# Kernel optimization log

Hardware: AMD Instinct MI355X
Metric: run time of the kernel (lower is better)

Reference implementation:

```python
import jax, jax.numpy as jnp
import numpy as np


def setup_inputs() -> dict:
    key = jax.random.key(0)
    k1, k2, k3, k4 = jax.random.split(key, 4)
    B, D_vis, E, N = 512, 4096, 1024, 512
    vf = jax.random.normal(k1, (B, D_vis), dtype=jnp.float32)
    p_lfs = jax.random.normal(k2, (B, E), dtype=jnp.float32)
    n_lfs = jax.random.normal(k3, (N, E), dtype=jnp.float32)
    W = jax.random.normal(k4, (E, D_vis), dtype=jnp.float32) * (1.0 / np.sqrt(D_vis))
    b = jnp.zeros((E,), dtype=jnp.float32)
    return {"vf": vf, "p_lfs": p_lfs, "n_lfs": n_lfs, "W": W, "b": b}


def _partial_order_sim(hypers, hypos):
    # -||relu(hypers - hypos)||_2 along last dim
    act = jax.nn.relu(hypers - hypos)
    return -jnp.sqrt(jnp.sum(act * act, axis=-1))


def reference(vf, p_lfs, n_lfs, W, b):
    # vf: [B, D_vis], W: [E, D_vis] -> vf_emb: [B, E]
    vf_emb = jnp.einsum("bd,ed->be", vf, W) + b
    # positive scores: [B]
    p_scores = _partial_order_sim(p_lfs, vf_emb)
    # negative scores, batched over B: n_lfs [N,E] vs vf_emb [B,E] -> [B,N]
    n_scores = _partial_order_sim(n_lfs[None, :, :], vf_emb[:, None, :])
    # score_stack: [B, 1+N]
    return jnp.concatenate([p_scores[:, None], n_scores], axis=1)
```

## Files before the change

kernel.cpp:

```cpp
#include <hip/hip_runtime.h>
#include <hip/hip_bf16.h>

constexpr int B = 512;
constexpr int D = 4096;
constexpr int E = 1024;
constexpr int N = 512;
constexpr int KSW = 16;
constexpr int KSG = 4;
constexpr int KC = D / KSW;
constexpr int NSTEP = KC / 32;
constexpr int ES = 8;
constexpr int EC = E / ES;
constexpr int DEPTH = 2;

typedef __attribute__((ext_vector_type(8))) short bf16x8;
typedef __attribute__((ext_vector_type(4))) float f32x4;
typedef _Float16 h2 __attribute__((ext_vector_type(2)));
typedef _Float16 h4 __attribute__((ext_vector_type(4)));
typedef _Float16 h8 __attribute__((ext_vector_type(8)));

typedef __attribute__((address_space(3))) void lds_void;
typedef const __attribute__((address_space(1))) void gbl_void;

__device__ __forceinline__ unsigned short f2bf(float f) {
    __hip_bfloat16 h = __float2bfloat16(f);
    return *reinterpret_cast<unsigned short*>(&h);
}

#if __has_builtin(__builtin_amdgcn_fdot2)
__device__ __forceinline__ float fdot2(h2 a, h2 b, float c) {
    return __builtin_amdgcn_fdot2(a, b, c, false);
}
#else
__device__ __forceinline__ float fdot2(h2 a, h2 b, float c) {
    return c + (float)a[0] * (float)b[0] + (float)a[1] * (float)b[1];
}
#endif

__global__ __launch_bounds__(256) void cvt_all(
    const float* __restrict__ vf, const float* __restrict__ W,
    const float* __restrict__ n_lfs,
    unsigned short* __restrict__ vfB, unsigned short* __restrict__ WB,
    _Float16* __restrict__ n16)
{
    const int bid = blockIdx.x;
    if (bid < 3072) {
        const float* src;
        unsigned short* dst;
        int i;
        if (bid < 1024) { src = vf; dst = vfB; i = (bid * 256 + threadIdx.x) * 8; }
        else           { src = W;  dst = WB;  i = ((bid - 1024) * 256 + threadIdx.x) * 8; }
        float4 v0 = *(const float4*)(src + i);
        float4 v1 = *(const float4*)(src + i + 4);
        bf16x8 o;
        o[0] = (short)f2bf(v0.x); o[1] = (short)f2bf(v0.y);
        o[2] = (short)f2bf(v0.z); o[3] = (short)f2bf(v0.w);
        o[4] = (short)f2bf(v1.x); o[5] = (short)f2bf(v1.y);
        o[6] = (short)f2bf(v1.z); o[7] = (short)f2bf(v1.w);
        *(bf16x8*)(dst + i) = o;
    } else {
        const int i = ((bid - 3072) * 256 + threadIdx.x) * 8;
        float4 v0 = *(const float4*)(n_lfs + i);
        float4 v1 = *(const float4*)(n_lfs + i + 4);
        h8 o;
        o[0] = (_Float16)v0.x; o[1] = (_Float16)v0.y;
        o[2] = (_Float16)v0.z; o[3] = (_Float16)v0.w;
        o[4] = (_Float16)v1.x; o[5] = (_Float16)v1.y;
        o[6] = (_Float16)v1.z; o[7] = (_Float16)v1.w;
        *(h8*)(n16 + i) = o;
    }
}

__global__ __launch_bounds__(256) void gemm_lds(
    const unsigned short* __restrict__ vf,
    const unsigned short* __restrict__ W,
    _Float16* __restrict__ part)
{
    __shared__ __align__(16) char smem[70656];

    const int t = threadIdx.x;
    const int w = t >> 6;
    const int L = t & 63;

    const int id = blockIdx.x + 16 * blockIdx.y + 128 * blockIdx.z;
    const int l  = (id & 7) * 64 + (id >> 3);
    const int z  = l >> 7;
    const int n0 = (l & 15) * 64;
    const int m0 = ((l >> 4) & 7) * 64;

    char* stg = smem + w * 16384;

    const int subrow = L >> 2;
    const int qstg = (L & 3) ^ ((L >> 2) & 3) ^ ((L >> 4) & 3);
    const int kbeg = (z * 4 + w) * KC;
    const unsigned short* aSrc[4];
    const unsigned short* bSrc[4];
    #pragma unroll
    for (int c = 0; c < 4; ++c) {
        aSrc[c] = vf + (size_t)(m0 + c * 16 + subrow) * D + kbeg + qstg * 8;
        bSrc[c] = W  + (size_t)(n0 + c * 16 + subrow) * D + kbeg + qstg * 8;
    }

    const int r16 = L & 15;
    const int quad = L >> 4;
    const int swz = quad ^ (r16 & 3) ^ ((r16 >> 2) & 3);
    const int aoff = r16 * 64 + swz * 16;

    f32x4 acc[4][4] = {};

    auto issue = [&](int step, int buf) {
        const size_t koff = (size_t)step * 32;
        #pragma unroll
        for (int c = 0; c < 4; ++c) {
            __builtin_amdgcn_global_load_lds(
                (gbl_void*)(aSrc[c] + koff),
                (lds_void*)(stg + buf * 4096 + c * 1024), 16, 0, 0);
            __builtin_amdgcn_global_load_lds(
                (gbl_void*)(bSrc[c] + koff),
                (lds_void*)(stg + 8192 + buf * 4096 + c * 1024), 16, 0, 0);
        }
    };

    issue(0, 0);
    issue(1, 1);

    #define GSTEP(S, WC, ISS)                                                  \
    {                                                                          \
        const int buf_ = (S) & 1;                                              \
        __builtin_amdgcn_s_waitcnt(WC);                                        \
        bf16x8 af[4], bg[4];                                                   \
        _Pragma("unroll")                                                      \
        for (int i = 0; i < 4; ++i)                                            \
            af[i] = *(const bf16x8*)(stg + buf_ * 4096 + i * 1024 + aoff);     \
        _Pragma("unroll")                                                      \
        for (int j = 0; j < 4; ++j)                                            \
            bg[j] = *(const bf16x8*)(stg + 8192 + buf_ * 4096 + j * 1024 + aoff); \
        _Pragma("unroll")                                                      \
        for (int i = 0; i < 4; ++i)                                            \
            _Pragma("unroll")                                                  \
            for (int j = 0; j < 4; ++j)                                        \
                acc[i][j] = __builtin_amdgcn_mfma_f32_16x16x32_bf16(           \
                    af[i], bg[j], acc[i][j], 0, 0, 0);                         \
        if (ISS) issue((S) + DEPTH, buf_);                                     \
    }

    #pragma unroll 1
    for (int s = 0; s < NSTEP - 1; ++s)
        GSTEP(s, 0x0F78, s + DEPTH < NSTEP);
    GSTEP(NSTEP - 1, 0x0F70, false);
    #undef GSTEP

    __syncthreads();
    float* ctw = (float*)smem + w * 4416;
    #pragma unroll
    for (int i = 0; i < 4; ++i)
        #pragma unroll
        for (int j = 0; j < 4; ++j)
            #pragma unroll
            for (int r = 0; r < 4; ++r)
                ctw[(i * 16 + quad * 4 + r) * 69 + (j * 16 + r16)] = acc[i][j][r];
    __syncthreads();

    const int row = t >> 2;
    const int cb  = (t & 3) * 16;
    const float* p0 = (const float*)smem + row * 69 + cb;
    float s[16];
    #pragma unroll
    for (int u = 0; u < 16; ++u)
        s[u] = (p0[u] + p0[4416 + u]) + (p0[8832 + u] + p0[13248 + u]);
    _Float16* po = part + (size_t)z * B * E + (size_t)(m0 + row) * E + n0 + cb;
    h8 v0, v1;
    #pragma unroll
    for (int u = 0; u < 8; ++u) { v0[u] = (_Float16)s[u]; v1[u] = (_Float16)s[u + 8]; }
    *(h8*)po = v0;
    *(h8*)(po + 8) = v1;
}

__global__ __launch_bounds__(256) void reduce_emb(
    const _Float16* __restrict__ part, const float* __restrict__ bias,
    const float* __restrict__ p_lfs,
    _Float16* __restrict__ emb16, float* __restrict__ out)
{
    const int b = blockIdx.x;
    const int e = threadIdx.x * 4;
    const size_t base = (size_t)b * E + e;
    float4 s = *(const float4*)(bias + e);
    #pragma unroll
    for (int ks = 0; ks < KSG; ++ks) {
        h4 p = *(const h4*)(part + (size_t)ks * B * E + base);
        s.x += (float)p[0]; s.y += (float)p[1];
        s.z += (float)p[2]; s.w += (float)p[3];
    }
    h4 o;
    o[0] = (_Float16)s.x; o[1] = (_Float16)s.y;
    o[2] = (_Float16)s.z; o[3] = (_Float16)s.w;
    *(h4*)(emb16 + base) = o;

    const float4 pl = *(const float4*)(p_lfs + base);
    float d, a = 0.f;
    d = pl.x - s.x; d = fmaxf(d, 0.f); a = fmaf(d, d, a);
    d = pl.y - s.y; d = fmaxf(d, 0.f); a = fmaf(d, d, a);
    d = pl.z - s.z; d = fmaxf(d, 0.f); a = fmaf(d, d, a);
    d = pl.w - s.w; d = fmaxf(d, 0.f); a = fmaf(d, d, a);
    #pragma unroll
    for (int off = 32; off; off >>= 1) a += __shfl_down(a, off, 64);
    __shared__ float red[4];
    if ((threadIdx.x & 63) == 0) red[threadIdx.x >> 6] = a;
    __syncthreads();
    if (threadIdx.x == 0)
        out[(size_t)b * 513] = -sqrtf(red[0] + red[1] + red[2] + red[3]);
}

__global__ __launch_bounds__(256, 4) void scores_part(
    const _Float16* __restrict__ emb16,
    const _Float16* __restrict__ n16,
    _Float16* __restrict__ pn)
{
    constexpr int LDH = EC + 8;
    __shared__ _Float16 eS[64 * LDH];
    __shared__ _Float16 nS[64 * LDH];

    const int t  = threadIdx.x;
    const int n0 = blockIdx.x * 64;
    const int b0 = blockIdx.y * 64;
    const int e0 = blockIdx.z * EC;

    {
        const int row = t >> 2;
        const int cb  = (t & 3) * 32;
        const _Float16* ep = emb16 + (size_t)(b0 + row) * E + e0 + cb;
        const _Float16* np = n16   + (size_t)(n0 + row) * E + e0 + cb;
        _Float16* ed = &eS[row * LDH + cb];
        _Float16* nd = &nS[row * LDH + cb];
        #pragma unroll
        for (int q = 0; q < 4; ++q) {
            h8 v = *(const h8*)(ep + q * 8);
            h8 w = *(const h8*)(np + q * 8);
            *(h8*)(ed + q * 8) = -v;
            *(h8*)(nd + q * 8) = w;
        }
    }
    __syncthreads();

    const int ty = t >> 4;
    const int tx = t & 15;

    float acc[4][4] = {};
    const h4 z4 = {};

    #pragma unroll 2
    for (int e = 0; e < EC; e += 4) {
        h4 a[4], c[4];
        #pragma unroll
        for (int r = 0; r < 4; ++r)
            a[r] = *(const h4*)&eS[(ty + 16 * r) * LDH + e];
        #pragma unroll
        for (int q = 0; q < 4; ++q)
            c[q] = *(const h4*)&nS[(tx + 16 * q) * LDH + e];
        #pragma unroll
        for (int r = 0; r < 4; ++r)
            #pragma unroll
            for (int q = 0; q < 4; ++q) {
                h4 d = c[q] + a[r];
                d = __builtin_elementwise_max(d, z4);
                h2 dl = __builtin_shufflevector(d, d, 0, 1);
                h2 dh = __builtin_shufflevector(d, d, 2, 3);
                acc[r][q] = fdot2(dl, dl, acc[r][q]);
                acc[r][q] = fdot2(dh, dh, acc[r][q]);
            }
    }

    _Float16* po = pn + (size_t)blockIdx.z * B * N;
    #pragma unroll
    for (int r = 0; r < 4; ++r) {
        const size_t ob = (size_t)(b0 + ty + 16 * r) * N;
        #pragma unroll
        for (int q = 0; q < 4; ++q)
            po[ob + n0 + tx + 16 * q] = (_Float16)acc[r][q];
    }
}

__global__ __launch_bounds__(256) void scores_final(
    const _Float16* __restrict__ pn,
    float* __restrict__ out)
{
    const int i = blockIdx.x * 256 + threadIdx.x;
    const int b = i >> 9;
    const int n = i & (N - 1);
    float s = 0.f;
    #pragma unroll
    for (int z = 0; z < ES; ++z)
        s += (float)pn[(size_t)z * B * N + i];
    out[(size_t)b * 513 + 1 + n] = -sqrtf(s);
}

extern "C" void kernel_launch(void* const* d_in, const int* in_sizes, int n_in,
                              void* d_out, int out_size, void* d_ws, size_t ws_size,
                              hipStream_t stream) {
    const float* vf    = (const float*)d_in[0];
    const float* p_lfs = (const float*)d_in[1];
    const float* n_lfs = (const float*)d_in[2];
    const float* W     = (const float*)d_in[3];
    const float* bias  = (const float*)d_in[4];
    float* out = (float*)d_out;

    char* ws = (char*)d_ws;
    _Float16*       pg    = (_Float16*)ws;
    _Float16*       pn    = (_Float16*)(ws + ((size_t)4 << 20));
    unsigned short* vfB   = (unsigned short*)(ws + ((size_t)8 << 20));
    unsigned short* WB    = (unsigned short*)(ws + ((size_t)12 << 20));
    _Float16*       emb16 = (_Float16*)(ws + ((size_t)20 << 20));
    _Float16*       n16   = (_Float16*)(ws + ((size_t)21 << 20));

    cvt_all<<<3328, 256, 0, stream>>>(vf, W, n_lfs, vfB, WB, n16);

    dim3 g1(E / 64, B / 64, KSG);
    gemm_lds<<<g1, 256, 0, stream>>>(vfB, WB, pg);

    reduce_emb<<<B, 256, 0, stream>>>(pg, bias, p_lfs, emb16, out);

    dim3 g3(N / 64, B / 64, ES);
    scores_part<<<g3, 256, 0, stream>>>(emb16, n16, pn);

    scores_final<<<(B * N) / 256, 256, 0, stream>>>(pn, out);
}
```

Measured before the change: 113.4 us.

## Fuse split-K reduction and positive scores into GEMM, convert n_lfs in scores kernel

```diff
diff --git a/kernel.cpp b/kernel.cpp
--- a/kernel.cpp
+++ b/kernel.cpp
@@ -5,9 +5,7 @@
 constexpr int D = 4096;
 constexpr int E = 1024;
 constexpr int N = 512;
-constexpr int KSW = 16;
-constexpr int KSG = 4;
-constexpr int KC = D / KSW;
+constexpr int KC = 512;
 constexpr int NSTEP = KC / 32;
 constexpr int ES = 8;
 constexpr int EC = E / ES;
@@ -39,86 +37,83 @@
 
 __global__ __launch_bounds__(256) void cvt_all(
     const float* __restrict__ vf, const float* __restrict__ W,
-    const float* __restrict__ n_lfs,
     unsigned short* __restrict__ vfB, unsigned short* __restrict__ WB,
-    _Float16* __restrict__ n16)
+    float* __restrict__ psum)
 {
     const int bid = blockIdx.x;
-    if (bid < 3072) {
-        const float* src;
-        unsigned short* dst;
-        int i;
-        if (bid < 1024) { src = vf; dst = vfB; i = (bid * 256 + threadIdx.x) * 8; }
-        else           { src = W;  dst = WB;  i = ((bid - 1024) * 256 + threadIdx.x) * 8; }
-        float4 v0 = *(const float4*)(src + i);
-        float4 v1 = *(const float4*)(src + i + 4);
-        bf16x8 o;
-        o[0] = (short)f2bf(v0.x); o[1] = (short)f2bf(v0.y);
-        o[2] = (short)f2bf(v0.z); o[3] = (short)f2bf(v0.w);
-        o[4] = (short)f2bf(v1.x); o[5] = (short)f2bf(v1.y);
-        o[6] = (short)f2bf(v1.z); o[7] = (short)f2bf(v1.w);
-        *(bf16x8*)(dst + i) = o;
-    } else {
-        const int i = ((bid - 3072) * 256 + threadIdx.x) * 8;
-        float4 v0 = *(const float4*)(n_lfs + i);
-        float4 v1 = *(const float4*)(n_lfs + i + 4);
-        h8 o;
-        o[0] = (_Float16)v0.x; o[1] = (_Float16)v0.y;
-        o[2] = (_Float16)v0.z; o[3] = (_Float16)v0.w;
-        o[4] = (_Float16)v1.x; o[5] = (_Float16)v1.y;
-        o[6] = (_Float16)v1.z; o[7] = (_Float16)v1.w;
-        *(h8*)(n16 + i) = o;
-    }
-}
-
-__global__ __launch_bounds__(256) void gemm_lds(
+    if (bid == 3072) {
+        if (threadIdx.x < 128)
+            ((f32x4*)psum)[threadIdx.x] = (f32x4){0.f, 0.f, 0.f, 0.f};
+        return;
+    }
+    const float* src;
+    unsigned short* dst;
+    int i;
+    if (bid < 1024) { src = vf; dst = vfB; i = (bid * 256 + threadIdx.x) * 8; }
+    else           { src = W;  dst = WB;  i = ((bid - 1024) * 256 + threadIdx.x) * 8; }
+    float4 v0 = *(const float4*)(src + i);
+    float4 v1 = *(const float4*)(src + i + 4);
+    bf16x8 o;
+    o[0] = (short)f2bf(v0.x); o[1] = (short)f2bf(v0.y);
+    o[2] = (short)f2bf(v0.z); o[3] = (short)f2bf(v0.w);
+    o[4] = (short)f2bf(v1.x); o[5] = (short)f2bf(v1.y);
+    o[6] = (short)f2bf(v1.z); o[7] = (short)f2bf(v1.w);
+    *(bf16x8*)(dst + i) = o;
+}
+
+__global__ __launch_bounds__(512, 2) void gemm_fused(
     const unsigned short* __restrict__ vf,
     const unsigned short* __restrict__ W,
-    _Float16* __restrict__ part)
+    const float* __restrict__ bias,
+    const float* __restrict__ p_lfs,
+    _Float16* __restrict__ emb16,
+    float* __restrict__ psum)
 {
-    __shared__ __align__(16) char smem[70656];
+    __shared__ __align__(16) char smem[98304];
 
     const int t = threadIdx.x;
     const int w = t >> 6;
     const int L = t & 63;
 
-    const int id = blockIdx.x + 16 * blockIdx.y + 128 * blockIdx.z;
-    const int l  = (id & 7) * 64 + (id >> 3);
-    const int z  = l >> 7;
-    const int n0 = (l & 15) * 64;
-    const int m0 = ((l >> 4) & 7) * 64;
-
-    char* stg = smem + w * 16384;
+    const int id  = blockIdx.x;
+    const int xcd = id & 7;
+    const int w8  = id >> 3;
+    const int m0 = ((xcd >> 2) * 8 + (w8 & 7)) * 32;
+    const int n0 = ((xcd & 3) * 4 + (w8 >> 3)) * 64;
+
+    char* stg = smem + w * 12288;
 
     const int subrow = L >> 2;
     const int qstg = (L & 3) ^ ((L >> 2) & 3) ^ ((L >> 4) & 3);
-    const int kbeg = (z * 4 + w) * KC;
-    const unsigned short* aSrc[4];
+    const int kbeg = w * KC;
+    const unsigned short* aSrc[2];
     const unsigned short* bSrc[4];
     #pragma unroll
-    for (int c = 0; c < 4; ++c) {
+    for (int c = 0; c < 2; ++c)
         aSrc[c] = vf + (size_t)(m0 + c * 16 + subrow) * D + kbeg + qstg * 8;
+    #pragma unroll
+    for (int c = 0; c < 4; ++c)
         bSrc[c] = W  + (size_t)(n0 + c * 16 + subrow) * D + kbeg + qstg * 8;
-    }
 
     const int r16 = L & 15;
     const int quad = L >> 4;
     const int swz = quad ^ (r16 & 3) ^ ((r16 >> 2) & 3);
     const int aoff = r16 * 64 + swz * 16;
 
-    f32x4 acc[4][4] = {};
+    f32x4 acc[2][4] = {};
 
     auto issue = [&](int step, int buf) {
         const size_t koff = (size_t)step * 32;
         #pragma unroll
-        for (int c = 0; c < 4; ++c) {
+        for (int c = 0; c < 2; ++c)
             __builtin_amdgcn_global_load_lds(
                 (gbl_void*)(aSrc[c] + koff),
-                (lds_void*)(stg + buf * 4096 + c * 1024), 16, 0, 0);
+                (lds_void*)(stg + buf * 2048 + c * 1024), 16, 0, 0);
+        #pragma unroll
+        for (int c = 0; c < 4; ++c)
             __builtin_amdgcn_global_load_lds(
                 (gbl_void*)(bSrc[c] + koff),
-                (lds_void*)(stg + 8192 + buf * 4096 + c * 1024), 16, 0, 0);
-        }
+                (lds_void*)(stg + 4096 + buf * 4096 + c * 1024), 16, 0, 0);
     };
 
     issue(0, 0);
@@ -128,15 +123,15 @@
     {                                                                          \
         const int buf_ = (S) & 1;                                              \
         __builtin_amdgcn_s_waitcnt(WC);                                        \
-        bf16x8 af[4], bg[4];                                                   \
+        bf16x8 af[2], bg[4];                                                   \
         _Pragma("unroll")                                                      \
-        for (int i = 0; i < 4; ++i)                                            \
-            af[i] = *(const bf16x8*)(stg + buf_ * 4096 + i * 1024 + aoff);     \
+        for (int i = 0; i < 2; ++i)                                            \
+            af[i] = *(const bf16x8*)(stg + buf_ * 2048 + i * 1024 + aoff);     \
         _Pragma("unroll")                                                      \
         for (int j = 0; j < 4; ++j)                                            \
-            bg[j] = *(const bf16x8*)(stg + 8192 + buf_ * 4096 + j * 1024 + aoff); \
+            bg[j] = *(const bf16x8*)(stg + 4096 + buf_ * 4096 + j * 1024 + aoff); \
         _Pragma("unroll")                                                      \
-        for (int i = 0; i < 4; ++i)                                            \
+        for (int i = 0; i < 2; ++i)                                            \
             _Pragma("unroll")                                                  \
             for (int j = 0; j < 4; ++j)                                        \
                 acc[i][j] = __builtin_amdgcn_mfma_f32_16x16x32_bf16(           \
@@ -146,14 +141,14 @@
 
     #pragma unroll 1
     for (int s = 0; s < NSTEP - 1; ++s)
-        GSTEP(s, 0x0F78, s + DEPTH < NSTEP);
+        GSTEP(s, 0x0F76, s + DEPTH < NSTEP);
     GSTEP(NSTEP - 1, 0x0F70, false);
     #undef GSTEP
 
     __syncthreads();
-    float* ctw = (float*)smem + w * 4416;
-    #pragma unroll
-    for (int i = 0; i < 4; ++i)
+    float* ctw = (float*)smem + w * 2208;
+    #pragma unroll
+    for (int i = 0; i < 2; ++i)
         #pragma unroll
         for (int j = 0; j < 4; ++j)
             #pragma unroll
@@ -161,59 +156,39 @@
                 ctw[(i * 16 + quad * 4 + r) * 69 + (j * 16 + r16)] = acc[i][j][r];
     __syncthreads();
 
-    const int row = t >> 2;
-    const int cb  = (t & 3) * 16;
-    const float* p0 = (const float*)smem + row * 69 + cb;
-    float s[16];
-    #pragma unroll
-    for (int u = 0; u < 16; ++u)
-        s[u] = (p0[u] + p0[4416 + u]) + (p0[8832 + u] + p0[13248 + u]);
-    _Float16* po = part + (size_t)z * B * E + (size_t)(m0 + row) * E + n0 + cb;
-    h8 v0, v1;
-    #pragma unroll
-    for (int u = 0; u < 8; ++u) { v0[u] = (_Float16)s[u]; v1[u] = (_Float16)s[u + 8]; }
-    *(h8*)po = v0;
-    *(h8*)(po + 8) = v1;
-}
-
-__global__ __launch_bounds__(256) void reduce_emb(
-    const _Float16* __restrict__ part, const float* __restrict__ bias,
-    const float* __restrict__ p_lfs,
-    _Float16* __restrict__ emb16, float* __restrict__ out)
-{
-    const int b = blockIdx.x;
-    const int e = threadIdx.x * 4;
-    const size_t base = (size_t)b * E + e;
-    float4 s = *(const float4*)(bias + e);
-    #pragma unroll
-    for (int ks = 0; ks < KSG; ++ks) {
-        h4 p = *(const h4*)(part + (size_t)ks * B * E + base);
-        s.x += (float)p[0]; s.y += (float)p[1];
-        s.z += (float)p[2]; s.w += (float)p[3];
-    }
+    const int row = t >> 4;
+    const int cb  = (t & 15) * 4;
+    const float* base = (const float*)smem + row * 69 + cb;
+    float s[4];
+    #pragma unroll
+    for (int u = 0; u < 4; ++u) {
+        float a01 = (base[u] + base[2208 + u]) + (base[4416 + u] + base[6624 + u]);
+        float a23 = (base[8832 + u] + base[11040 + u]) + (base[13248 + u] + base[15456 + u]);
+        s[u] = a01 + a23;
+    }
+    const float4 bl = *(const float4*)(bias + n0 + cb);
+    s[0] += bl.x; s[1] += bl.y; s[2] += bl.z; s[3] += bl.w;
+
+    const size_t obase = (size_t)(m0 + row) * E + n0 + cb;
     h4 o;
-    o[0] = (_Float16)s.x; o[1] = (_Float16)s.y;
-    o[2] = (_Float16)s.z; o[3] = (_Float16)s.w;
-    *(h4*)(emb16 + base) = o;
-
-    const float4 pl = *(const float4*)(p_lfs + base);
+    o[0] = (_Float16)s[0]; o[1] = (_Float16)s[1];
+    o[2] = (_Float16)s[2]; o[3] = (_Float16)s[3];
+    *(h4*)(emb16 + obase) = o;
+
+    const float4 pl = *(const float4*)(p_lfs + obase);
     float d, a = 0.f;
-    d = pl.x - s.x; d = fmaxf(d, 0.f); a = fmaf(d, d, a);
-    d = pl.y - s.y; d = fmaxf(d, 0.f); a = fmaf(d, d, a);
-    d = pl.z - s.z; d = fmaxf(d, 0.f); a = fmaf(d, d, a);
-    d = pl.w - s.w; d = fmaxf(d, 0.f); a = fmaf(d, d, a);
-    #pragma unroll
-    for (int off = 32; off; off >>= 1) a += __shfl_down(a, off, 64);
-    __shared__ float red[4];
-    if ((threadIdx.x & 63) == 0) red[threadIdx.x >> 6] = a;
-    __syncthreads();
-    if (threadIdx.x == 0)
-        out[(size_t)b * 513] = -sqrtf(red[0] + red[1] + red[2] + red[3]);
+    d = pl.x - s[0]; d = fmaxf(d, 0.f); a = fmaf(d, d, a);
+    d = pl.y - s[1]; d = fmaxf(d, 0.f); a = fmaf(d, d, a);
+    d = pl.z - s[2]; d = fmaxf(d, 0.f); a = fmaf(d, d, a);
+    d = pl.w - s[3]; d = fmaxf(d, 0.f); a = fmaf(d, d, a);
+    #pragma unroll
+    for (int off = 8; off; off >>= 1) a += __shfl_down(a, off, 16);
+    if ((t & 15) == 0) atomicAdd(psum + m0 + row, a);
 }
 
 __global__ __launch_bounds__(256, 4) void scores_part(
     const _Float16* __restrict__ emb16,
-    const _Float16* __restrict__ n16,
+    const float* __restrict__ n_lfs,
     _Float16* __restrict__ pn)
 {
     constexpr int LDH = EC + 8;
@@ -229,15 +204,21 @@
         const int row = t >> 2;
         const int cb  = (t & 3) * 32;
         const _Float16* ep = emb16 + (size_t)(b0 + row) * E + e0 + cb;
-        const _Float16* np = n16   + (size_t)(n0 + row) * E + e0 + cb;
+        const float*    np = n_lfs + (size_t)(n0 + row) * E + e0 + cb;
         _Float16* ed = &eS[row * LDH + cb];
         _Float16* nd = &nS[row * LDH + cb];
         #pragma unroll
         for (int q = 0; q < 4; ++q) {
             h8 v = *(const h8*)(ep + q * 8);
-            h8 w = *(const h8*)(np + q * 8);
+            float4 w0 = *(const float4*)(np + q * 8);
+            float4 w1 = *(const float4*)(np + q * 8 + 4);
+            h8 wv;
+            wv[0] = (_Float16)w0.x; wv[1] = (_Float16)w0.y;
+            wv[2] = (_Float16)w0.z; wv[3] = (_Float16)w0.w;
+            wv[4] = (_Float16)w1.x; wv[5] = (_Float16)w1.y;
+            wv[6] = (_Float16)w1.z; wv[7] = (_Float16)w1.w;
             *(h8*)(ed + q * 8) = -v;
-            *(h8*)(nd + q * 8) = w;
+            *(h8*)(nd + q * 8) = wv;
         }
     }
     __syncthreads();
@@ -282,8 +263,14 @@
 
 __global__ __launch_bounds__(256) void scores_final(
     const _Float16* __restrict__ pn,
+    const float* __restrict__ psum,
     float* __restrict__ out)
 {
+    if (blockIdx.x >= 1024) {
+        const int idx = (blockIdx.x - 1024) * 256 + threadIdx.x;
+        out[(size_t)idx * 513] = -sqrtf(psum[idx]);
+        return;
+    }
     const int i = blockIdx.x * 256 + threadIdx.x;
     const int b = i >> 9;
     const int n = i & (N - 1);
@@ -305,22 +292,18 @@
     float* out = (float*)d_out;
 
     char* ws = (char*)d_ws;
-    _Float16*       pg    = (_Float16*)ws;
-    _Float16*       pn    = (_Float16*)(ws + ((size_t)4 << 20));
-    unsigned short* vfB   = (unsigned short*)(ws + ((size_t)8 << 20));
-    unsigned short* WB    = (unsigned short*)(ws + ((size_t)12 << 20));
-    _Float16*       emb16 = (_Float16*)(ws + ((size_t)20 << 20));
-    _Float16*       n16   = (_Float16*)(ws + ((size_t)21 << 20));
-
-    cvt_all<<<3328, 256, 0, stream>>>(vf, W, n_lfs, vfB, WB, n16);
-
-    dim3 g1(E / 64, B / 64, KSG);
-    gemm_lds<<<g1, 256, 0, stream>>>(vfB, WB, pg);
-
-    reduce_emb<<<B, 256, 0, stream>>>(pg, bias, p_lfs, emb16, out);
+    _Float16*       pn    = (_Float16*)ws;
+    unsigned short* vfB   = (unsigned short*)(ws + ((size_t)4 << 20));
+    unsigned short* WB    = (unsigned short*)(ws + ((size_t)8 << 20));
+    _Float16*       emb16 = (_Float16*)(ws + ((size_t)16 << 20));
+    float*          psum  = (float*)(ws + ((size_t)17 << 20));
+
+    cvt_all<<<3073, 256, 0, stream>>>(vf, W, vfB, WB, psum);
+
+    gemm_fused<<<256, 512, 0, stream>>>(vfB, WB, bias, p_lfs, emb16, psum);
 
     dim3 g3(N / 64, B / 64, ES);
-    scores_part<<<g3, 256, 0, stream>>>(emb16, n16, pn);
-
-    scores_final<<<(B * N) / 256, 256, 0, stream>>>(pn, out);
-}
+    scores_part<<<g3, 256, 0, stream>>>(emb16, n_lfs, pn);
+
+    scores_final<<<1026, 256, 0, stream>>>(pn, psum, out);
+}
```

New measurement: 115.7 us. +2.1%, slower.

## Fuse split-E score partials and final reduction into one double-buffered kernel

Applied to the files above, without the earlier changes.

```diff
diff --git a/kernel.cpp b/kernel.cpp
--- a/kernel.cpp
+++ b/kernel.cpp
@@ -211,87 +211,77 @@
         out[(size_t)b * 513] = -sqrtf(red[0] + red[1] + red[2] + red[3]);
 }
 
-__global__ __launch_bounds__(256, 4) void scores_part(
+__global__ __launch_bounds__(256, 2) void scores_fused(
     const _Float16* __restrict__ emb16,
     const _Float16* __restrict__ n16,
-    _Float16* __restrict__ pn)
-{
-    constexpr int LDH = EC + 8;
-    __shared__ _Float16 eS[64 * LDH];
-    __shared__ _Float16 nS[64 * LDH];
-
-    const int t  = threadIdx.x;
-    const int n0 = blockIdx.x * 64;
-    const int b0 = blockIdx.y * 64;
-    const int e0 = blockIdx.z * EC;
-
-    {
-        const int row = t >> 2;
-        const int cb  = (t & 3) * 32;
-        const _Float16* ep = emb16 + (size_t)(b0 + row) * E + e0 + cb;
-        const _Float16* np = n16   + (size_t)(n0 + row) * E + e0 + cb;
-        _Float16* ed = &eS[row * LDH + cb];
-        _Float16* nd = &nS[row * LDH + cb];
-        #pragma unroll
-        for (int q = 0; q < 4; ++q) {
-            h8 v = *(const h8*)(ep + q * 8);
-            h8 w = *(const h8*)(np + q * 8);
-            *(h8*)(ed + q * 8) = -v;
-            *(h8*)(nd + q * 8) = w;
-        }
-    }
-    __syncthreads();
-
-    const int ty = t >> 4;
-    const int tx = t & 15;
-
-    float acc[4][4] = {};
-    const h4 z4 = {};
-
-    #pragma unroll 2
-    for (int e = 0; e < EC; e += 4) {
-        h4 a[4], c[4];
-        #pragma unroll
-        for (int r = 0; r < 4; ++r)
-            a[r] = *(const h4*)&eS[(ty + 16 * r) * LDH + e];
-        #pragma unroll
-        for (int q = 0; q < 4; ++q)
-            c[q] = *(const h4*)&nS[(tx + 16 * q) * LDH + e];
-        #pragma unroll
-        for (int r = 0; r < 4; ++r)
-            #pragma unroll
-            for (int q = 0; q < 4; ++q) {
-                h4 d = c[q] + a[r];
-                d = __builtin_elementwise_max(d, z4);
-                h2 dl = __builtin_shufflevector(d, d, 0, 1);
-                h2 dh = __builtin_shufflevector(d, d, 2, 3);
-                acc[r][q] = fdot2(dl, dl, acc[r][q]);
-                acc[r][q] = fdot2(dh, dh, acc[r][q]);
-            }
-    }
-
-    _Float16* po = pn + (size_t)blockIdx.z * B * N;
-    #pragma unroll
-    for (int r = 0; r < 4; ++r) {
-        const size_t ob = (size_t)(b0 + ty + 16 * r) * N;
-        #pragma unroll
-        for (int q = 0; q < 4; ++q)
-            po[ob + n0 + tx + 16 * q] = (_Float16)acc[r][q];
-    }
-}
-
-__global__ __launch_bounds__(256) void scores_final(
-    const _Float16* __restrict__ pn,
     float* __restrict__ out)
 {
-    const int i = blockIdx.x * 256 + threadIdx.x;
-    const int b = i >> 9;
-    const int n = i & (N - 1);
-    float s = 0.f;
-    #pragma unroll
-    for (int z = 0; z < ES; ++z)
-        s += (float)pn[(size_t)z * B * N + i];
-    out[(size_t)b * 513 + 1 + n] = -sqrtf(s);
+    constexpr int SB = 16, SN = 32;
+    constexpr int LDHE = 136;
+    constexpr int LDHN = 140;
+
+    __shared__ _Float16 eS[2][SB * LDHE];
+    __shared__ _Float16 nS[2][SN * LDHN];
+
+    const int t  = threadIdx.x;
+    const int n0 = blockIdx.x * SN;
+    const int b0 = blockIdx.y * SB;
+
+    const int er = t >> 4;
+    const int ec = (t & 15) * 8;
+    const int nr = t >> 3;
+    const int nc = (t & 7) * 16;
+
+    auto stage = [&](int c, int buf) {
+        const int e0 = c * EC;
+        h8 v = *(const h8*)(emb16 + (size_t)(b0 + er) * E + e0 + ec);
+        *(h8*)&eS[buf][er * LDHE + ec] = -v;
+        h8 w0 = *(const h8*)(n16 + (size_t)(n0 + nr) * E + e0 + nc);
+        h8 w1 = *(const h8*)(n16 + (size_t)(n0 + nr) * E + e0 + nc + 8);
+        _Float16* nd = &nS[buf][nr * LDHN + nc];
+        *(h4*)(nd)      = __builtin_shufflevector(w0, w0, 0, 1, 2, 3);
+        *(h4*)(nd + 4)  = __builtin_shufflevector(w0, w0, 4, 5, 6, 7);
+        *(h4*)(nd + 8)  = __builtin_shufflevector(w1, w1, 0, 1, 2, 3);
+        *(h4*)(nd + 12) = __builtin_shufflevector(w1, w1, 4, 5, 6, 7);
+    };
+
+    const int tx = t & 31;
+    const int ty = t >> 5;
+
+    float acc0 = 0.f, acc1 = 0.f;
+    const h4 z4 = {};
+
+    stage(0, 0);
+    __syncthreads();
+
+    #pragma unroll 1
+    for (int c = 0; c < ES; ++c) {
+        const int buf = c & 1;
+        if (c + 1 < ES) stage(c + 1, buf ^ 1);
+
+        #pragma unroll 4
+        for (int e = 0; e < EC; e += 4) {
+            h4 a0 = *(const h4*)&eS[buf][ty * LDHE + e];
+            h4 a1 = *(const h4*)&eS[buf][(ty + 8) * LDHE + e];
+            h4 cc = *(const h4*)&nS[buf][tx * LDHN + e];
+            h4 d0 = cc + a0;
+            h4 d1 = cc + a1;
+            d0 = __builtin_elementwise_max(d0, z4);
+            d1 = __builtin_elementwise_max(d1, z4);
+            h2 d0l = __builtin_shufflevector(d0, d0, 0, 1);
+            h2 d0h = __builtin_shufflevector(d0, d0, 2, 3);
+            h2 d1l = __builtin_shufflevector(d1, d1, 0, 1);
+            h2 d1h = __builtin_shufflevector(d1, d1, 2, 3);
+            acc0 = fdot2(d0l, d0l, acc0);
+            acc0 = fdot2(d0h, d0h, acc0);
+            acc1 = fdot2(d1l, d1l, acc1);
+            acc1 = fdot2(d1h, d1h, acc1);
+        }
+        __syncthreads();
+    }
+
+    out[(size_t)(b0 + ty) * 513 + 1 + n0 + tx]     = -sqrtf(acc0);
+    out[(size_t)(b0 + ty + 8) * 513 + 1 + n0 + tx] = -sqrtf(acc1);
 }
 
 extern "C" void kernel_launch(void* const* d_in, const int* in_sizes, int n_in,
@@ -306,11 +296,10 @@
 
     char* ws = (char*)d_ws;
     _Float16*       pg    = (_Float16*)ws;
-    _Float16*       pn    = (_Float16*)(ws + ((size_t)4 << 20));
-    unsigned short* vfB   = (unsigned short*)(ws + ((size_t)8 << 20));
-    unsigned short* WB    = (unsigned short*)(ws + ((size_t)12 << 20));
-    _Float16*       emb16 = (_Float16*)(ws + ((size_t)20 << 20));
-    _Float16*       n16   = (_Float16*)(ws + ((size_t)21 << 20));
+    unsigned short* vfB   = (unsigned short*)(ws + ((size_t)4 << 20));
+    unsigned short* WB    = (unsigned short*)(ws + ((size_t)8 << 20));
+    _Float16*       emb16 = (_Float16*)(ws + ((size_t)16 << 20));
+    _Float16*       n16   = (_Float16*)(ws + ((size_t)17 << 20));
 
     cvt_all<<<3328, 256, 0, stream>>>(vf, W, n_lfs, vfB, WB, n16);
 
@@ -319,8 +308,6 @@
 
     reduce_emb<<<B, 256, 0, stream>>>(pg, bias, p_lfs, emb16, out);
 
-    dim3 g3(N / 64, B / 64, ES);
-    scores_part<<<g3, 256, 0, stream>>>(emb16, n16, pn);
-
-    scores_final<<<(B * N) / 256, 256, 0, stream>>>(pn, out);
-}
+    dim3 g3(N / 32, B / 16);
+    scores_fused<<<g3, 256, 0, stream>>>(emb16, n16, out);
+}
```

After: 115.4 us. Within noise of the previous version (+1.7%).
